# Kernel optimization log

Hardware: AMD Instinct MI355X
Metric: run time of the kernel (lower is better)

Reference implementation:

```python
import jax, jax.numpy as jnp
import numpy as np

INPUT_DIM = 246
HIDDEN = 512
OUTPUT_DIM = 123
B, T = 128, 500
N_DIFF, N_ABIL = 11, 8


def setup_inputs() -> dict:
    key = jax.random.key(0)
    ks = jax.random.split(key, 9)
    feats = jax.random.normal(ks[0], (B, T, INPUT_DIM), dtype=jnp.float32)
    ability = jax.random.randint(ks[1], (B, T, 1), 0, N_ABIL).astype(jnp.float32)
    diff = jax.random.randint(ks[2], (B, T, 1), 0, N_DIFF).astype(jnp.float32)
    x = jnp.concatenate([feats, ability, diff], axis=-1)  # [B,T,248]
    in_dim = INPUT_DIM + N_DIFF + N_ABIL  # 265
    s_ih = 1.0 / np.sqrt(HIDDEN)
    W_ih = jax.random.uniform(ks[3], (4 * HIDDEN, in_dim), jnp.float32, -s_ih, s_ih)
    W_hh = jax.random.uniform(ks[4], (4 * HIDDEN, HIDDEN), jnp.float32, -s_ih, s_ih)
    b_ih = jax.random.uniform(ks[5], (4 * HIDDEN,), jnp.float32, -s_ih, s_ih)
    b_hh = jax.random.uniform(ks[6], (4 * HIDDEN,), jnp.float32, -s_ih, s_ih)
    s_fc = 1.0 / np.sqrt(HIDDEN)
    W_fc = jax.random.uniform(ks[7], (OUTPUT_DIM, HIDDEN), jnp.float32, -s_fc, s_fc)
    b_fc = jax.random.uniform(ks[8], (OUTPUT_DIM,), jnp.float32, -s_fc, s_fc)
    return {"x": x, "W_ih": W_ih, "W_hh": W_hh, "b_ih": b_ih, "b_hh": b_hh,
            "W_fc": W_fc, "b_fc": b_fc}


def _lstm(x, W_ih, W_hh, b_ih, b_hh):
    # x: [B,T,In] -> out: [B,T,H]; PyTorch gate order i,f,g,o
    Bsz = x.shape[0]
    H = W_hh.shape[1]
    x_proj = jnp.einsum('bti,gi->btg', x, W_ih) + b_ih + b_hh  # [B,T,4H]

    def step(carry, xt):
        h, c = carry
        gates = xt + h @ W_hh.T
        i, f, g, o = jnp.split(gates, 4, axis=-1)
        i, f, o = jax.nn.sigmoid(i), jax.nn.sigmoid(f), jax.nn.sigmoid(o)
        g = jnp.tanh(g)
        c = f * c + i * g
        h = o * jnp.tanh(c)
        return (h, c), h

    h0 = jnp.zeros((Bsz, H), x.dtype)
    c0 = jnp.zeros((Bsz, H), x.dtype)
    (_, _), hs = jax.lax.scan(step, (h0, c0), x_proj.transpose(1, 0, 2))
    return hs.transpose(1, 0, 2)


def reference(x, W_ih, W_hh, b_ih, b_hh, W_fc, b_fc):
    feats = x[..., :INPUT_DIM]
    ability = x[..., -2].astype(jnp.int32)
    diff = x[..., -1].astype(jnp.int32)
    one_hot_diff = jax.nn.one_hot(diff, N_DIFF, dtype=x.dtype)
    one_hot_ab = jax.nn.one_hot(ability, N_ABIL, dtype=x.dtype)
    new_x = jnp.tanh(jnp.concatenate([feats, one_hot_diff, one_hot_ab], axis=-1))
    out = _lstm(new_x, W_ih, W_hh, b_ih, b_hh)  # [B,T,H]
    res = jax.nn.sigmoid(jnp.einsum('bth,oh->bto', out, W_fc) + b_fc)
    return res[:, :-1, :]
```

## Files before the change

### kernel.cpp

```cpp
#include <hip/hip_runtime.h>
#include <hip/hip_fp16.h>


typedef _Float16 f16;
typedef _Float16 f16x8 __attribute__((ext_vector_type(8)));
typedef float f32x4 __attribute__((ext_vector_type(4)));
typedef unsigned u32x4 __attribute__((ext_vector_type(4)));

#define TS 499

#define NEWX_OFF   0ul
#define NEWX_BYTES (500ul*8*9216)
#define HALL_OFF   (NEWX_OFF + NEWX_BYTES)
#define HALL_BYTES (500ul*128*512*2)
#define WHH_OFF    (HALL_OFF + HALL_BYTES)
#define WHH_BYTES  (2048ul*512*2)
#define WIH_OFF    (WHH_OFF + WHH_BYTES)
#define WIH_BYTES  (2048ul*288*2)
#define WFC_OFF    (WIH_OFF + WIH_BYTES)
#define WFC_BYTES  (128ul*512*2)
#define BIAS_OFF   (WFC_OFF + WFC_BYTES)
#define BIAS_BYTES (2048ul*4)
#define CNT_OFF    (BIAS_OFF + BIAS_BYTES)
#define CNT_BYTES  (8192ul)
#define WS_NEED    (CNT_OFF + CNT_BYTES)

__device__ __forceinline__ float tanh_dev(float x) {
    float ax = fabsf(x);
    float e  = __expf(-2.f * ax);
    float r  = (1.f - e) / (1.f + e);
    return copysignf(r, x);
}
__device__ __forceinline__ float sigm_dev(float x) {
    float e = __expf(-fabsf(x));
    float p = 1.f / (1.f + e);
    return x >= 0.f ? p : 1.f - p;
}

__device__ __forceinline__ void llc_store_nowait(unsigned* p, unsigned v) {
    asm volatile("global_store_dword %0, %1, off sc0 sc1" :: "v"(p), "v"(v) : "memory");
}
__device__ __forceinline__ unsigned llc_load_u32(const unsigned* p) {
    unsigned v;
    asm volatile("global_load_dword %0, %1, off sc0 sc1\n\ts_waitcnt vmcnt(0)"
                 : "=v"(v) : "v"(p) : "memory");
    return v;
}

__global__ void __launch_bounds__(256) prep_newx(const float* __restrict__ x,
                                                 f16* __restrict__ newx) {
    const int t  = blockIdx.x;
    const int bt = blockIdx.y;
    const int tid = threadIdx.x;
    char* tb = (char*)newx + ((size_t)t * 8 + bt) * 9216;
    for (int idx = tid; idx < 16 * 288; idx += 256) {
        const int r = idx / 288, k = idx - r * 288;
        const float* xr = x + ((size_t)(bt * 16 + r) * 500 + t) * 248;
        float v;
        if (k < 246)      v = tanh_dev(xr[k]);
        else if (k < 257) v = (k - 246 == (int)xr[247]) ? 0.76159415595576485f : 0.f;
        else if (k < 265) v = (k - 257 == (int)xr[246]) ? 0.76159415595576485f : 0.f;
        else              v = 0.f;
        const int col8 = k >> 3;
        const int byte = (col8 >> 2) * 1024 + (((col8 & 3) * 16 + r) << 4) + ((k & 7) << 1);
        *(f16*)(tb + byte) = (f16)v;
    }
}

__global__ void __launch_bounds__(256) prep_w(const float* __restrict__ W_ih,
                                              const float* __restrict__ W_hh,
                                              const float* __restrict__ W_fc,
                                              const float* __restrict__ b_ih,
                                              const float* __restrict__ b_hh,
                                              f16* __restrict__ whh, f16* __restrict__ wih,
                                              f16* __restrict__ wfc, float* __restrict__ bias) {
    const int NHH = 2048 * 512;
    const int NIH = 2048 * 288;
    const int NFC = 128 * 512;
    const int NT  = NHH + NIH + NFC + 2048;
    for (int i = blockIdx.x * 256 + threadIdx.x; i < NT; i += gridDim.x * 256) {
        if (i < NHH) {
            whh[i] = (f16)W_hh[i];
        } else if (i < NHH + NIH) {
            int j2 = i - NHH; int rr = j2 / 288, kk = j2 % 288;
            wih[j2] = (kk < 265) ? (f16)W_ih[rr * 265 + kk] : (f16)0.f;
        } else if (i < NHH + NIH + NFC) {
            int j2 = i - (NHH + NIH); int rr = j2 >> 9, kk = j2 & 511;
            wfc[j2] = (rr < 123) ? (f16)W_fc[rr * 512 + kk] : (f16)0.f;
        } else {
            int j2 = i - (NHH + NIH + NFC);
            bias[j2] = b_ih[j2] + b_hh[j2];
        }
    }
}

__global__ void __launch_bounds__(512, 1) lstm_seq(const f16* __restrict__ newx_,
                                                   f16* __restrict__ hall,
                                                   const f16* __restrict__ whh,
                                                   const f16* __restrict__ wih,
                                                   const float* __restrict__ bias,
                                                   unsigned* __restrict__ cnt) {
    __shared__ __align__(16) char hsb[16 * 1024];
    __shared__ float gf[4 * 560];
    __shared__ __align__(16) f16 hout[512];
    __shared__ volatile int tok;

    const char* newx = (const char*)newx_;
    const int tid = threadIdx.x, bid = blockIdx.x;
    const int btile = bid & 7;
    const int hsl   = bid >> 3;

    const int w = tid >> 6, wl = tid & 63;
    const int arow = wl & 15, kgrp = wl >> 4;
    const int g = w & 3, cb = w >> 2;
    const int grow = g * 512 + hsl * 32 + cb * 16 + arow;
    const int bE = tid >> 5, colE = tid & 31;

    f16x8 wh[16], wi[9];
    #pragma unroll
    for (int kc = 0; kc < 16; ++kc)
        wh[kc] = *(const f16x8*)(whh + (size_t)grow * 512 + kc * 32 + kgrp * 8);
    #pragma unroll
    for (int kc = 0; kc < 9; ++kc)
        wi[kc] = *(const f16x8*)(wih + (size_t)grow * 288 + kc * 32 + kgrp * 8);
    const float bb = bias[grow];

    unsigned* const flags  = cnt + btile * 256;
    unsigned* const myflag = flags + hsl * 16;

    const int srow = tid & 15, sc8 = tid >> 4;
    const int soff1 = (sc8 >> 2) * 1024 + (((sc8 & 3) * 16 + srow) << 4);
    const int soff2 = soff1 + 8 * 1024;

    float c_st = 0.f;

    f16x8 xa[9];
    {
        const char* xt = newx + (size_t)btile * 9216;
        #pragma unroll
        for (int kc = 0; kc < 9; ++kc)
            xa[kc] = *(const f16x8*)(xt + kc * 1024 + wl * 16);
    }

    if (tid == 0) tok = 0;
    __syncthreads();

    for (int t = 0; t < TS; ++t) {
        f32x4 acc = {bb, bb, bb, bb};
        #pragma unroll
        for (int kc = 0; kc < 9; ++kc)
            acc = __builtin_amdgcn_mfma_f32_16x16x32_f16(xa[kc], wi[kc], acc, 0, 0, 0);
        {
            const char* xt1 = newx + ((size_t)(t + 1) * 8 + btile) * 9216;
            #pragma unroll
            for (int kc = 0; kc < 9; ++kc)
                xa[kc] = *(const f16x8*)(xt1 + kc * 1024 + wl * 16);
        }

        if (t > 0) {
            if (tid < 64) {
                int spins = 0;
                for (;;) {
                    unsigned f = (unsigned)t;
                    if (wl < 16) f = llc_load_u32(flags + wl * 16);
                    if (__ballot(f >= (unsigned)t) == ~0ull) break;
                    __builtin_amdgcn_s_sleep(1);
                    if (++spins > (1 << 15)) break;
                }
                if (tid == 0) tok = t;
            } else {
                int spins = 0;
                while (tok < t) {
                    __builtin_amdgcn_s_sleep(1);
                    if (++spins > (1 << 17)) break;
                }
            }
            {
                const char* hb = (const char*)hall + ((size_t)(t - 1) * 128 + btile * 16) * 1024;
                const char* ga1 = hb + srow * 1024 + sc8 * 16;
                const char* ga2 = ga1 + 512;
                u32x4 h0, h1;
                asm volatile("global_load_dwordx4 %0, %2, off sc0 sc1\n\t"
                             "global_load_dwordx4 %1, %3, off sc0 sc1\n\t"
                             "s_waitcnt vmcnt(0)"
                             : "=&v"(h0), "=&v"(h1) : "v"(ga1), "v"(ga2) : "memory");
                *(u32x4*)(hsb + soff1) = h0;
                *(u32x4*)(hsb + soff2) = h1;
            }
            __syncthreads();

            f32x4 e0 = {0.f,0.f,0.f,0.f}, e1 = {0.f,0.f,0.f,0.f};
            #pragma unroll
            for (int kc = 0; kc < 16; kc += 2) {
                f16x8 a0 = *(const f16x8*)(hsb + kc * 1024 + wl * 16);
                f16x8 a1 = *(const f16x8*)(hsb + (kc + 1) * 1024 + wl * 16);
                e0 = __builtin_amdgcn_mfma_f32_16x16x32_f16(a0, wh[kc],     e0, 0, 0, 0);
                e1 = __builtin_amdgcn_mfma_f32_16x16x32_f16(a1, wh[kc + 1], e1, 0, 0, 0);
            }
            acc += e0; acc += e1;
        }

        {
            float* gp = gf + g * 560 + cb * 16 + (wl & 15);
            const int b4 = (wl >> 4) * 4;
            gp[(b4 + 0) * 35] = acc[0];
            gp[(b4 + 1) * 35] = acc[1];
            gp[(b4 + 2) * 35] = acc[2];
            gp[(b4 + 3) * 35] = acc[3];
        }
        __syncthreads();

        {
            const float* gq = gf + bE * 35 + colE;
            float iv = sigm_dev(gq[0]);
            float fv = sigm_dev(gq[560]);
            float gv = tanh_dev(gq[1120]);
            float ov = sigm_dev(gq[1680]);
            c_st = fv * c_st + iv * gv;
            float hv = ov * tanh_dev(c_st);
            hout[bE * 32 + colE] = (f16)hv;
        }
        __syncthreads();

        if ((tid >> 6) == (t & 7)) {
            u32x4 hv4 = *(const u32x4*)((const char*)hout + wl * 16);
            const f16* sp = hall + ((size_t)t * 128 + btile * 16 + (wl >> 2)) * 512
                            + hsl * 32 + (wl & 3) * 8;
            asm volatile("global_store_dwordx4 %0, %1, off sc0 sc1\n\t"
                         "s_waitcnt vmcnt(0)"
                         :: "v"(sp), "v"(hv4) : "memory");
            if (wl == 0) llc_store_nowait(myflag, (unsigned)(t + 1));
        }
    }
}

__global__ void __launch_bounds__(256) out_gemm(const f16* __restrict__ hall,
                                                const f16* __restrict__ wfc,
                                                const float* __restrict__ bfc,
                                                float* __restrict__ out) {
    const int tid = threadIdx.x;
    const int w = tid >> 6, wl = tid & 63;
    const int arow = wl & 15, kgrp = wl >> 4;
    const long m0 = (long)blockIdx.x * 64 + w * 16;
    const f16* ap = hall + (m0 + arow) * 512 + kgrp * 8;
    f16x8 a[16];
    #pragma unroll
    for (int kc = 0; kc < 16; ++kc) a[kc] = *(const f16x8*)(ap + kc * 32);
    #pragma unroll
    for (int jt = 0; jt < 8; ++jt) {
        f32x4 acc = {0.f, 0.f, 0.f, 0.f};
        const f16* bp = wfc + (size_t)(jt * 16 + arow) * 512 + kgrp * 8;
        #pragma unroll
        for (int kc = 0; kc < 16; ++kc)
            acc = __builtin_amdgcn_mfma_f32_16x16x32_f16(a[kc], *(const f16x8*)(bp + kc * 32),
                                                         acc, 0, 0, 0);
        const int col = jt * 16 + arow;
        if (col < 123) {
            const float bv = bfc[col];
            #pragma unroll
            for (int rr = 0; rr < 4; ++rr) {
                long m = m0 + kgrp * 4 + rr;
                int tt = (int)(m >> 7), b = (int)(m & 127);
                out[((size_t)b * 499 + tt) * 123 + col] = sigm_dev(acc[rr] + bv);
            }
        }
    }
}

extern "C" void kernel_launch(void* const* d_in, const int* in_sizes, int n_in,
                              void* d_out, int out_size, void* d_ws, size_t ws_size,
                              hipStream_t stream) {
    if (ws_size < WS_NEED) return;

    const float* x    = (const float*)d_in[0];
    const float* W_ih = (const float*)d_in[1];
    const float* W_hh = (const float*)d_in[2];
    const float* b_ih = (const float*)d_in[3];
    const float* b_hh = (const float*)d_in[4];
    const float* W_fc = (const float*)d_in[5];
    const float* b_fc = (const float*)d_in[6];
    float* out = (float*)d_out;
    char* ws = (char*)d_ws;

    f16* newx   = (f16*)(ws + NEWX_OFF);
    f16* hall   = (f16*)(ws + HALL_OFF);
    f16* whh    = (f16*)(ws + WHH_OFF);
    f16* wih    = (f16*)(ws + WIH_OFF);
    f16* wfc    = (f16*)(ws + WFC_OFF);
    float* bias = (float*)(ws + BIAS_OFF);
    unsigned* cnt = (unsigned*)(ws + CNT_OFF);

    (void)hipMemsetAsync(cnt, 0, CNT_BYTES, stream);

    prep_newx<<<dim3(TS, 8), 256, 0, stream>>>(x, newx);
    prep_w<<<512, 256, 0, stream>>>(W_ih, W_hh, W_fc, b_ih, b_hh, whh, wih, wfc, bias);

    void* args[6] = {&newx, &hall, &whh, &wih, &bias, &cnt};
    (void)hipLaunchCooperativeKernel((const void*)lstm_seq, dim3(128), dim3(512), args,
                                     0, stream);

    out_gemm<<<998, 256, 0, stream>>>(hall, wfc, b_fc, out);
}
```

Before: 1.486 ms.

## Replace flag-based inter-block sync with sentinel-filled hidden-state polling

Drops the per-timestep flag counters and the two-level wave spin/token handshake. The hidden-state buffer is now pre-filled with 0xFF as a NaN sentinel, and each thread polls its own h slice until no sentinel halves remain. This removes the flag store, the store-completion wait and the extra round trip before reading h. The cost is a 65 MB memset every call. It also risks a hang or stale data if a real fp16 value equals 0xFFFF, which is mitigated by a timeout and a scrub step. The cooperative launch is replaced by a plain launch.

```diff
diff --git a/kernel.cpp b/kernel.cpp
--- a/kernel.cpp
+++ b/kernel.cpp
@@ -21,9 +21,7 @@
 #define WFC_BYTES  (128ul*512*2)
 #define BIAS_OFF   (WFC_OFF + WFC_BYTES)
 #define BIAS_BYTES (2048ul*4)
-#define CNT_OFF    (BIAS_OFF + BIAS_BYTES)
-#define CNT_BYTES  (8192ul)
-#define WS_NEED    (CNT_OFF + CNT_BYTES)
+#define WS_NEED    (BIAS_OFF + BIAS_BYTES)
 
 __device__ __forceinline__ float tanh_dev(float x) {
     float ax = fabsf(x);
@@ -35,16 +33,6 @@
     float e = __expf(-fabsf(x));
     float p = 1.f / (1.f + e);
     return x >= 0.f ? p : 1.f - p;
-}
-
-__device__ __forceinline__ void llc_store_nowait(unsigned* p, unsigned v) {
-    asm volatile("global_store_dword %0, %1, off sc0 sc1" :: "v"(p), "v"(v) : "memory");
-}
-__device__ __forceinline__ unsigned llc_load_u32(const unsigned* p) {
-    unsigned v;
-    asm volatile("global_load_dword %0, %1, off sc0 sc1\n\ts_waitcnt vmcnt(0)"
-                 : "=v"(v) : "v"(p) : "memory");
-    return v;
 }
 
 __global__ void __launch_bounds__(256) prep_newx(const float* __restrict__ x,
@@ -94,16 +82,32 @@
     }
 }
 
+#define CHKU16(H) { u32x4 _u = __builtin_bit_cast(u32x4, H);                  \
+    bad |= (unsigned)((_u[0] >> 16) == 0xFFFFu) | (unsigned)((_u[0] & 0xFFFFu) == 0xFFFFu); \
+    bad |= (unsigned)((_u[1] >> 16) == 0xFFFFu) | (unsigned)((_u[1] & 0xFFFFu) == 0xFFFFu); \
+    bad |= (unsigned)((_u[2] >> 16) == 0xFFFFu) | (unsigned)((_u[2] & 0xFFFFu) == 0xFFFFu); \
+    bad |= (unsigned)((_u[3] >> 16) == 0xFFFFu) | (unsigned)((_u[3] & 0xFFFFu) == 0xFFFFu); }
+
+__device__ __forceinline__ u32x4 scrub(u32x4 h) {
+    u32x4 u = h;
+    #pragma unroll
+    for (int i = 0; i < 4; ++i) {
+        unsigned v = u[i];
+        if ((v & 0xFFFFu) == 0xFFFFu) v &= 0xFFFF0000u;
+        if ((v >> 16)     == 0xFFFFu) v &= 0x0000FFFFu;
+        u[i] = v;
+    }
+    return u;
+}
+
 __global__ void __launch_bounds__(512, 1) lstm_seq(const f16* __restrict__ newx_,
                                                    f16* __restrict__ hall,
                                                    const f16* __restrict__ whh,
                                                    const f16* __restrict__ wih,
-                                                   const float* __restrict__ bias,
-                                                   unsigned* __restrict__ cnt) {
+                                                   const float* __restrict__ bias) {
     __shared__ __align__(16) char hsb[16 * 1024];
     __shared__ float gf[4 * 560];
     __shared__ __align__(16) f16 hout[512];
-    __shared__ volatile int tok;
 
     const char* newx = (const char*)newx_;
     const int tid = threadIdx.x, bid = blockIdx.x;
@@ -124,9 +128,6 @@
     for (int kc = 0; kc < 9; ++kc)
         wi[kc] = *(const f16x8*)(wih + (size_t)grow * 288 + kc * 32 + kgrp * 8);
     const float bb = bias[grow];
-
-    unsigned* const flags  = cnt + btile * 256;
-    unsigned* const myflag = flags + hsl * 16;
 
     const int srow = tid & 15, sc8 = tid >> 4;
     const int soff1 = (sc8 >> 2) * 1024 + (((sc8 & 3) * 16 + srow) << 4);
@@ -141,9 +142,6 @@
         for (int kc = 0; kc < 9; ++kc)
             xa[kc] = *(const f16x8*)(xt + kc * 1024 + wl * 16);
     }
-
-    if (tid == 0) tok = 0;
-    __syncthreads();
 
     for (int t = 0; t < TS; ++t) {
         f32x4 acc = {bb, bb, bb, bb};
@@ -158,35 +156,26 @@
         }
 
         if (t > 0) {
-            if (tid < 64) {
-                int spins = 0;
-                for (;;) {
-                    unsigned f = (unsigned)t;
-                    if (wl < 16) f = llc_load_u32(flags + wl * 16);
-                    if (__ballot(f >= (unsigned)t) == ~0ull) break;
-                    __builtin_amdgcn_s_sleep(1);
-                    if (++spins > (1 << 15)) break;
-                }
-                if (tid == 0) tok = t;
-            } else {
-                int spins = 0;
-                while (tok < t) {
-                    __builtin_amdgcn_s_sleep(1);
-                    if (++spins > (1 << 17)) break;
-                }
-            }
-            {
-                const char* hb = (const char*)hall + ((size_t)(t - 1) * 128 + btile * 16) * 1024;
-                const char* ga1 = hb + srow * 1024 + sc8 * 16;
-                const char* ga2 = ga1 + 512;
-                u32x4 h0, h1;
+            const char* hb = (const char*)hall + ((size_t)(t - 1) * 128 + btile * 16) * 1024;
+            const char* ga1 = hb + srow * 1024 + sc8 * 16;
+            const char* ga2 = ga1 + 512;
+            u32x4 h0, h1;
+            int spins = 0;
+            bool timeout = false;
+            for (;;) {
                 asm volatile("global_load_dwordx4 %0, %2, off sc0 sc1\n\t"
                              "global_load_dwordx4 %1, %3, off sc0 sc1\n\t"
                              "s_waitcnt vmcnt(0)"
                              : "=&v"(h0), "=&v"(h1) : "v"(ga1), "v"(ga2) : "memory");
-                *(u32x4*)(hsb + soff1) = h0;
-                *(u32x4*)(hsb + soff2) = h1;
+                unsigned bad = 0;
+                CHKU16(h0); CHKU16(h1);
+                if (__ballot(bad) == 0ull) break;
+                if (++spins > 4096) { timeout = true; break; }
+                if (spins > 2) __builtin_amdgcn_s_sleep(4);
             }
+            if (timeout) { h0 = scrub(h0); h1 = scrub(h1); }
+            *(u32x4*)(hsb + soff1) = h0;
+            *(u32x4*)(hsb + soff2) = h1;
             __syncthreads();
 
             f32x4 e0 = {0.f,0.f,0.f,0.f}, e1 = {0.f,0.f,0.f,0.f};
@@ -226,10 +215,8 @@
             u32x4 hv4 = *(const u32x4*)((const char*)hout + wl * 16);
             const f16* sp = hall + ((size_t)t * 128 + btile * 16 + (wl >> 2)) * 512
                             + hsl * 32 + (wl & 3) * 8;
-            asm volatile("global_store_dwordx4 %0, %1, off sc0 sc1\n\t"
-                         "s_waitcnt vmcnt(0)"
+            asm volatile("global_store_dwordx4 %0, %1, off sc0 sc1"
                          :: "v"(sp), "v"(hv4) : "memory");
-            if (wl == 0) llc_store_nowait(myflag, (unsigned)(t + 1));
         }
     }
 }
@@ -288,16 +275,13 @@
     f16* wih    = (f16*)(ws + WIH_OFF);
     f16* wfc    = (f16*)(ws + WFC_OFF);
     float* bias = (float*)(ws + BIAS_OFF);
-    unsigned* cnt = (unsigned*)(ws + CNT_OFF);
-
-    (void)hipMemsetAsync(cnt, 0, CNT_BYTES, stream);
+
+    (void)hipMemsetAsync(hall, 0xFF, HALL_BYTES, stream);
 
     prep_newx<<<dim3(TS, 8), 256, 0, stream>>>(x, newx);
     prep_w<<<512, 256, 0, stream>>>(W_ih, W_hh, W_fc, b_ih, b_hh, whh, wih, wfc, bias);
 
-    void* args[6] = {&newx, &hall, &whh, &wih, &bias, &cnt};
-    (void)hipLaunchCooperativeKernel((const void*)lstm_seq, dim3(128), dim3(512), args,
-                                     0, stream);
+    lstm_seq<<<dim3(128), dim3(512), 0, stream>>>(newx, hall, whh, wih, bias);
 
     out_gemm<<<998, 256, 0, stream>>>(hall, wfc, b_fc, out);
 }
```

New measurement: 1.260 ms. 15.2% less time.
